# Optimization experiments

Hardware: AMD Instinct MI355X
Metric: run time of the kernel (lower is better)

Reference implementation:

```python
import jax, jax.numpy as jnp
import numpy as np

WS = 7            # window size
HEADS = 4
DIM = 128         # hidden_dim
HEAD_DIM = 128    # wrapper passes head_dim=hidden_dim (faithful to source)
INNER = HEADS * HEAD_DIM   # 512
MLP = 4 * DIM
PATCH = 4
DISP = WS // 2
NEG = -1e9


def _ln(x, g, b, eps=1e-5):
    m = jnp.mean(x, -1, keepdims=True)
    v = jnp.mean((x - m) ** 2, -1, keepdims=True)
    return (x - m) * jax.lax.rsqrt(v + eps) * g + b


_coords = np.stack(np.meshgrid(np.arange(WS), np.arange(WS), indexing='ij'), -1).reshape(-1, 2)
REL_IDX = jnp.asarray(_coords[None] - _coords[:, None] + WS - 1)  # (ws^2, ws^2, 2)


def _build_masks():
    n = WS * WS
    ul = np.zeros((n, n), np.float32)
    ul[-DISP * WS:, : -DISP * WS] = NEG
    ul[: -DISP * WS, -DISP * WS:] = NEG
    lr = np.zeros((WS, WS, WS, WS), np.float32)
    lr[:, -DISP:, :, : -DISP] = NEG
    lr[:, : -DISP, :, -DISP:] = NEG
    return jnp.asarray(ul), jnp.asarray(lr.reshape(n, n))

UL_MASK, LR_MASK = _build_masks()


def _win_attn(x, w_qkv, pos, w_o, b_o, shifted):
    b, H, W, _ = x.shape
    if shifted:
        x = jnp.roll(x, (-DISP, -DISP), axis=(1, 2))
    nh, nw = H // WS, W // WS
    qkv = x @ w_qkv  # (b, H, W, 3*INNER)

    def to_win(t):  # -> (b, heads, n_windows, ws*ws, head_dim)
        t = t.reshape(b, nh, WS, nw, WS, HEADS, HEAD_DIM)
        return t.transpose(0, 5, 1, 3, 2, 4, 6).reshape(b, HEADS, nh * nw, WS * WS, HEAD_DIM)

    q, k, v = map(to_win, jnp.split(qkv, 3, axis=-1))
    dots = jnp.einsum('bhwid,bhwjd->bhwij', q, k) * (HEAD_DIM ** -0.5)
    dots = dots + pos[REL_IDX[..., 0], REL_IDX[..., 1]]  # shared across heads (berniwal)
    if shifted:
        dots = dots.at[:, :, -nw:].add(UL_MASK)
        dots = dots.at[:, :, nw - 1::nw].add(LR_MASK)
    attn = jax.nn.softmax(dots, axis=-1)
    out = jnp.einsum('bhwij,bhwjd->bhwid', attn, v)
    out = out.reshape(b, HEADS, nh, nw, WS, WS, HEAD_DIM).transpose(0, 2, 4, 3, 5, 1, 6)
    out = out.reshape(b, H, W, INNER) @ w_o + b_o
    if shifted:
        out = jnp.roll(out, (DISP, DISP), axis=(1, 2))
    return out


def _block(x, ga1, be1, w_qkv, pos, w_o, b_o, ga2, be2, w1, b1, w2, b2, shifted):
    x = x + _win_attn(_ln(x, ga1, be1), w_qkv, pos, w_o, b_o, shifted)
    h = jax.nn.gelu(_ln(x, ga2, be2) @ w1 + b1, approximate=False) @ w2 + b2
    return x + h


def _patch_embed(x, w, b):  # Unfold(patch) + Linear, channel-major feature order
    B, C, H, W = x.shape
    nh, nw = H // PATCH, W // PATCH
    x = x.reshape(B, C, nh, PATCH, nw, PATCH).transpose(0, 2, 4, 1, 3, 5)
    return x.reshape(B, nh, nw, C * PATCH * PATCH) @ w + b


def setup_inputs() -> dict:
    key = jax.random.key(0)
    ks = iter(jax.random.split(key, 48))

    def nrm(shape, s=0.02):
        return jax.random.normal(next(ks), shape, dtype=jnp.float32) * s

    inp = {'x': jax.random.normal(next(ks), (32, 3, 224, 224), dtype=jnp.float32)}
    inp['w_pe'] = nrm((3 * PATCH * PATCH, DIM))
    inp['b_pe'] = jnp.zeros((DIM,), jnp.float32)
    for s in ('a', 'b'):
        inp['ga1_' + s] = jnp.ones((DIM,), jnp.float32)
        inp['be1_' + s] = jnp.zeros((DIM,), jnp.float32)
        inp['w_qkv_' + s] = nrm((DIM, 3 * INNER))
        inp['pos_' + s] = nrm((2 * WS - 1, 2 * WS - 1), 1.0)
        inp['w_o_' + s] = nrm((INNER, DIM))
        inp['b_o_' + s] = jnp.zeros((DIM,), jnp.float32)
        inp['ga2_' + s] = jnp.ones((DIM,), jnp.float32)
        inp['be2_' + s] = jnp.zeros((DIM,), jnp.float32)
        inp['w_m1_' + s] = nrm((DIM, MLP))
        inp['b_m1_' + s] = jnp.zeros((MLP,), jnp.float32)
        inp['w_m2_' + s] = nrm((MLP, DIM))
        inp['b_m2_' + s] = jnp.zeros((DIM,), jnp.float32)
    return inp


def reference(x, w_pe, b_pe,
              ga1_a, be1_a, w_qkv_a, pos_a, w_o_a, b_o_a, ga2_a, be2_a, w_m1_a, b_m1_a, w_m2_a, b_m2_a,
              ga1_b, be1_b, w_qkv_b, pos_b, w_o_b, b_o_b, ga2_b, be2_b, w_m1_b, b_m1_b, w_m2_b, b_m2_b):
    h = _patch_embed(x, w_pe, b_pe)  # (B, 56, 56, DIM)
    h = _block(h, ga1_a, be1_a, w_qkv_a, pos_a, w_o_a, b_o_a, ga2_a, be2_a, w_m1_a, b_m1_a, w_m2_a, b_m2_a, False)
    h = _block(h, ga1_b, be1_b, w_qkv_b, pos_b, w_o_b, b_o_b, ga2_b, be2_b, w_m1_b, b_m1_b, w_m2_b, b_m2_b, True)
    return h
```

## Files before the change

kernel.cpp:

```cpp
#include <hip/hip_runtime.h>

typedef __attribute__((ext_vector_type(8))) short bf16x8;
typedef __attribute__((ext_vector_type(4))) short bf16x4;
typedef __attribute__((ext_vector_type(4))) float f32x4;
typedef __attribute__((ext_vector_type(2))) unsigned u32x2;

#define MFMA16(a, b, c) __builtin_amdgcn_mfma_f32_16x16x32_bf16(a, b, c, 0, 0, 0)

static __device__ __forceinline__ short f2bf(float f) {
    union { float f; unsigned u; } x; x.f = f;
    unsigned r = x.u + 0x7FFFu + ((x.u >> 16) & 1u);
    return (short)(r >> 16);
}

static __device__ __forceinline__ unsigned cvtpk(float lo, float hi) {
    unsigned r;
    asm("v_cvt_pk_bf16_f32 %0, %1, %2" : "=v"(r) : "v"(lo), "v"(hi));
    return r;
}

static __device__ __forceinline__ void gload16(const void* g, void* l) {
    __builtin_amdgcn_global_load_lds((const __attribute__((address_space(1))) void*)g,
                                     (__attribute__((address_space(3))) void*)l, 16, 0, 0);
}

__global__ void wconv_kernel(const float* __restrict__ i_qkv, const float* __restrict__ i_o,
                             const float* __restrict__ i_m1, const float* __restrict__ i_m2,
                             short* __restrict__ wqkv, short* __restrict__ wo,
                             short* __restrict__ wm1, short* __restrict__ wm2) {
    int idx = blockIdx.x * 256 + threadIdx.x;
    if (idx < 196608) {
        int k = idx & 127, n = idx >> 7;
        wqkv[idx] = f2bf(i_qkv[k * 1536 + n]);
    } else if (idx < 262144) {
        int l = idx - 196608; int k = l & 511, n = l >> 9;
        wo[l] = f2bf(i_o[k * 128 + n]);
    } else if (idx < 327680) {
        int l = idx - 262144; int k = l & 127, n = l >> 7;
        wm1[l] = f2bf(i_m1[k * 512 + n]);
    } else {
        int l = idx - 327680; int k = l & 511, n = l >> 9;
        wm2[l] = f2bf(i_m2[k * 128 + n]);
    }
}

__global__ void tabgen_kernel(const float* __restrict__ pos_a, const float* __restrict__ pos_b,
                              float* __restrict__ tab) {
    int v = blockIdx.x;
    const float* pos = (v == 0) ? pos_a : pos_b;
    for (int e = threadIdx.x; e < 4096; e += 256) {
        int row = e >> 6, key = e & 63;
        float val;
        if (key >= 49) val = -1e9f;
        else if (row >= 49) val = 0.f;
        else {
            int qi = row / 7, qj = row - qi * 7, ki = key / 7, kj = key - ki * 7;
            val = pos[(ki - qi + 6) * 13 + (kj - qj + 6)];
            if (v >= 1) {
                bool wh7 = (v - 1) & 2, ww7 = (v - 1) & 1;
                if (wh7 && ((qi >= 4) != (ki >= 4))) val += -1e9f;
                if (ww7 && ((qj >= 4) != (kj >= 4))) val += -1e9f;
            }
        }
        tab[v * 4096 + e] = val;
    }
}

__global__ __launch_bounds__(256) void patchln_kernel(const float* __restrict__ x,
                                                      const float* __restrict__ w,
                                                      const float* __restrict__ bias,
                                                      const float* __restrict__ g,
                                                      const float* __restrict__ bta,
                                                      float* __restrict__ out,
                                                      short* __restrict__ xn) {
    __shared__ float s_in[2][48];
    __shared__ float red[2][2][2];
    const int tid = threadIdx.x;
    const int half = tid >> 7, c = tid & 127;
    const int winh = (tid >> 6) & 1, lane = tid & 63;
    const int t = blockIdx.x * 2 + half;
    const int b = t / 3136, rem = t - b * 3136;
    const int hp = rem / 56, wp = rem - hp * 56;
    if (c < 48) {
        int cin = c >> 4, py = (c >> 2) & 3, px = c & 3;
        s_in[half][c] = x[((size_t)(b * 3 + cin) * 224 + hp * 4 + py) * 224 + wp * 4 + px];
    }
    __syncthreads();
    float acc = bias[c];
#pragma unroll
    for (int k = 0; k < 48; ++k) acc += s_in[half][k] * w[k * 128 + c];
    out[(size_t)t * 128 + c] = acc;
    float s1 = acc, s2 = acc * acc;
#pragma unroll
    for (int o = 32; o > 0; o >>= 1) { s1 += __shfl_xor(s1, o); s2 += __shfl_xor(s2, o); }
    if (lane == 0) { red[half][winh][0] = s1; red[half][winh][1] = s2; }
    __syncthreads();
    s1 = red[half][0][0] + red[half][1][0];
    s2 = red[half][0][1] + red[half][1][1];
    float mean = s1 * (1.f / 128.f);
    float var = s2 * (1.f / 128.f) - mean * mean;
    float rstd = rsqrtf(var + 1e-5f);
    xn[(size_t)t * 128 + c] = f2bf((acc - mean) * rstd * g[c] + bta[c]);
}

template <int SHIFTED>
__global__ __launch_bounds__(256, 3) void attn_kernel(const short* __restrict__ xn,
                                                      const short* __restrict__ wqkvT,
                                                      const float* __restrict__ tab,
                                                      const short* __restrict__ zpad,
                                                      short* __restrict__ aout) {
    __shared__ short smem[24576];
    short* s_x = smem;
    short* s_q = smem + 8192;
    short* s_k = smem + 16384;
    short* s_vT = smem + 8192;
    short* s_p = smem + 16384;

    const int tid = threadIdx.x;
    const int wid = tid >> 6, lane = tid & 63;
    const int l15 = lane & 15, l4 = lane >> 4, klo = l4 * 8;
    const int bid = blockIdx.x;
    const int win = bid & 63, head = (bid >> 6) & 3, b = bid >> 8;
    const int wh = win >> 3, ww = win & 7;

#pragma unroll
    for (int it = 0; it < 4; ++it) {
        int slot = it * 256 + tid;
        int row = slot >> 4, scol = slot & 15;
        int colb = (scol * 16) ^ ((row & 7) << 4);
        const char* g;
        if (row < 49) {
            int wi = (row * 37) >> 8, wj = row - wi * 7;
            int hh = wh * 7 + wi, wp = ww * 7 + wj;
            if (SHIFTED) { hh += 3; if (hh >= 56) hh -= 56; wp += 3; if (wp >= 56) wp -= 56; }
            int t = (b * 56 + hh) * 56 + wp;
            g = (const char*)(xn + (size_t)t * 128) + colb;
        } else {
            g = (const char*)zpad + colb;
        }
        gload16(g, (char*)smem + (it * 256 + wid * 64) * 16);
    }
    __syncthreads();

    const f32x4 zero4 = {0.f, 0.f, 0.f, 0.f};

    {
        const short* Wq = wqkvT + (size_t)(head * 128) * 128;
        const short* Wk = wqkvT + (size_t)(512 + head * 128) * 128;
        f32x4 aq[2][4], ak[2][4];
#pragma unroll
        for (int mw = 0; mw < 2; ++mw)
#pragma unroll
            for (int j = 0; j < 4; ++j) { aq[mw][j] = zero4; ak[mw][j] = zero4; }
#pragma unroll
        for (int k0 = 0; k0 < 4; ++k0) {
            bf16x8 bx[4], awq[2], awk[2];
#pragma unroll
            for (int j = 0; j < 4; ++j) {
                int row = j * 16 + l15;
                bx[j] = *(const bf16x8*)((const char*)s_x + row * 256 + ((k0 * 64 + l4 * 16) ^ ((row & 7) << 4)));
            }
#pragma unroll
            for (int mw = 0; mw < 2; ++mw) {
                awq[mw] = *(const bf16x8*)(Wq + (size_t)(wid * 32 + mw * 16 + l15) * 128 + k0 * 32 + klo);
                awk[mw] = *(const bf16x8*)(Wk + (size_t)(wid * 32 + mw * 16 + l15) * 128 + k0 * 32 + klo);
            }
            __builtin_amdgcn_s_setprio(1);
#pragma unroll
            for (int mw = 0; mw < 2; ++mw)
#pragma unroll
                for (int j = 0; j < 4; ++j) {
                    aq[mw][j] = MFMA16(awq[mw], bx[j], aq[mw][j]);
                    ak[mw][j] = MFMA16(awk[mw], bx[j], ak[mw][j]);
                }
            __builtin_amdgcn_s_setprio(0);
        }
#pragma unroll
        for (int mw = 0; mw < 2; ++mw)
#pragma unroll
            for (int j = 0; j < 4; ++j) {
                u32x2 pq = { cvtpk(aq[mw][j][0], aq[mw][j][1]), cvtpk(aq[mw][j][2], aq[mw][j][3]) };
                u32x2 pk = { cvtpk(ak[mw][j][0], ak[mw][j][1]), cvtpk(ak[mw][j][2], ak[mw][j][3]) };
                int row = j * 16 + l15;
                int colb = (wid * 64 + mw * 32 + l4 * 8) ^ ((row & 7) << 4);
                *(u32x2*)((char*)s_q + row * 256 + colb) = pq;
                *(u32x2*)((char*)s_k + row * 256 + colb) = pk;
            }
    }
    __syncthreads();

    const int qrow = wid * 16 + l15;
    f32x4 dt[4];
#pragma unroll
    for (int m = 0; m < 4; ++m) dt[m] = zero4;
#pragma unroll
    for (int k0 = 0; k0 < 4; ++k0) {
        bf16x8 bq = *(const bf16x8*)((const char*)s_q + qrow * 256 + ((k0 * 64 + l4 * 16) ^ ((qrow & 7) << 4)));
        __builtin_amdgcn_s_setprio(1);
#pragma unroll
        for (int m = 0; m < 4; ++m) {
            int krow = m * 16 + l15;
            bf16x8 akf = *(const bf16x8*)((const char*)s_k + krow * 256 + ((k0 * 64 + l4 * 16) ^ ((krow & 7) << 4)));
            dt[m] = MFMA16(akf, bq, dt[m]);
        }
        __builtin_amdgcn_s_setprio(0);
    }
    __syncthreads();

    const int variant = SHIFTED ? (1 + ((wh == 7) ? 2 : 0) + ((ww == 7) ? 1 : 0)) : 0;
    const float* tv = tab + variant * 4096 + qrow * 64;
    const float SC = 0.08838834764831845f;
    float p[4][4];
    float mx = -3.0e38f;
#pragma unroll
    for (int m = 0; m < 4; ++m) {
        f32x4 tb = *(const f32x4*)(tv + m * 16 + l4 * 4);
#pragma unroll
        for (int r = 0; r < 4; ++r) {
            float d = dt[m][r] * SC + tb[r];
            p[m][r] = d;
            mx = fmaxf(mx, d);
        }
    }
    mx = fmaxf(mx, __shfl_xor(mx, 16));
    mx = fmaxf(mx, __shfl_xor(mx, 32));
    float sum = 0.f;
#pragma unroll
    for (int m = 0; m < 4; ++m)
#pragma unroll
        for (int r = 0; r < 4; ++r) { p[m][r] = __expf(p[m][r] - mx); sum += p[m][r]; }
    sum += __shfl_xor(sum, 16);
    sum += __shfl_xor(sum, 32);
    float inv = 1.f / sum;
#pragma unroll
    for (int m = 0; m < 4; ++m) {
        u32x2 pv = { cvtpk(p[m][0] * inv, p[m][1] * inv), cvtpk(p[m][2] * inv, p[m][3] * inv) };
        *(u32x2*)((char*)s_p + qrow * 128 + ((m * 32 + l4 * 8) ^ ((qrow & 7) << 4))) = pv;
    }

    {
        const short* Wv = wqkvT + (size_t)(1024 + head * 128) * 128;
        f32x4 acc[4][2];
#pragma unroll
        for (int m = 0; m < 4; ++m)
#pragma unroll
            for (int n = 0; n < 2; ++n) acc[m][n] = zero4;
#pragma unroll
        for (int k0 = 0; k0 < 4; ++k0) {
            bf16x8 ax[4], bw[2];
#pragma unroll
            for (int m = 0; m < 4; ++m) {
                int row = m * 16 + l15;
                ax[m] = *(const bf16x8*)((const char*)s_x + row * 256 + ((k0 * 64 + l4 * 16) ^ ((row & 7) << 4)));
            }
#pragma unroll
            for (int n = 0; n < 2; ++n)
                bw[n] = *(const bf16x8*)(Wv + (size_t)(wid * 32 + n * 16 + l15) * 128 + k0 * 32 + klo);
            __builtin_amdgcn_s_setprio(1);
#pragma unroll
            for (int m = 0; m < 4; ++m)
#pragma unroll
                for (int n = 0; n < 2; ++n) acc[m][n] = MFMA16(ax[m], bw[n], acc[m][n]);
            __builtin_amdgcn_s_setprio(0);
        }
#pragma unroll
        for (int m = 0; m < 4; ++m)
#pragma unroll
            for (int n = 0; n < 2; ++n) {
                u32x2 pv = { cvtpk(acc[m][n][0], acc[m][n][1]), cvtpk(acc[m][n][2], acc[m][n][3]) };
                int hd = wid * 32 + n * 16 + l15;
                *(u32x2*)((char*)s_vT + hd * 128 + ((m * 32 + l4 * 8) ^ ((hd & 7) << 4))) = pv;
            }
    }
    __syncthreads();

    f32x4 o[4][2];
#pragma unroll
    for (int m = 0; m < 4; ++m)
#pragma unroll
        for (int n = 0; n < 2; ++n) o[m][n] = zero4;
#pragma unroll
    for (int k0 = 0; k0 < 2; ++k0) {
        bf16x8 ap[4], bv[2];
#pragma unroll
        for (int m = 0; m < 4; ++m) {
            int row = m * 16 + l15;
            ap[m] = *(const bf16x8*)((const char*)s_p + row * 128 + ((k0 * 64 + l4 * 16) ^ ((row & 7) << 4)));
        }
#pragma unroll
        for (int n = 0; n < 2; ++n) {
            int hd = wid * 32 + n * 16 + l15;
            bv[n] = *(const bf16x8*)((const char*)s_vT + hd * 128 + ((k0 * 64 + l4 * 16) ^ ((hd & 7) << 4)));
        }
        __builtin_amdgcn_s_setprio(1);
#pragma unroll
        for (int m = 0; m < 4; ++m)
#pragma unroll
            for (int n = 0; n < 2; ++n) o[m][n] = MFMA16(ap[m], bv[n], o[m][n]);
        __builtin_amdgcn_s_setprio(0);
    }
#pragma unroll
    for (int m = 0; m < 4; ++m) {
#pragma unroll
        for (int r = 0; r < 4; ++r) {
            int rl = m * 16 + l4 * 4 + r;
            if (rl < 49) {
                int wi = (rl * 37) >> 8, wj = rl - wi * 7;
                int hh = wh * 7 + wi, wp = ww * 7 + wj;
                if (SHIFTED) { hh += 3; if (hh >= 56) hh -= 56; wp += 3; if (wp >= 56) wp -= 56; }
                size_t t = (size_t)(b * 56 + hh) * 56 + wp;
                aout[t * 512 + head * 128 + wid * 32 + l15] = f2bf(o[m][0][r]);
                aout[t * 512 + head * 128 + wid * 32 + 16 + l15] = f2bf(o[m][1][r]);
            }
        }
    }
}

template <int K, int MODE>
__global__ __launch_bounds__(256, 2) void gemm4_kernel(const short* __restrict__ A,
                                                       const short* __restrict__ BT,
                                                       const float* __restrict__ bias,
                                                       const float* __restrict__ resid,
                                                       const float* __restrict__ g,
                                                       const float* __restrict__ bta,
                                                       float* __restrict__ outf,
                                                       short* __restrict__ outb,
                                                       int Ntot) {
    __shared__ char smem[65536];
    float* red = (float*)smem;

    const int tid = threadIdx.x, wid = tid >> 6, lane = tid & 63;
    const int wr = wid >> 1, wc = wid & 1;
    const int l15 = lane & 15, l4 = lane >> 4;
    const int m0 = blockIdx.x * 128;
    const int nb0 = blockIdx.y * 128;

    auto stage = [&](int kc, int bi) {
#pragma unroll
        for (int it = 0; it < 4; ++it) {
            int slot = it * 256 + tid;
            int row = slot >> 3, scol = slot & 7;
            int colb = (scol * 16) ^ ((row & 7) << 4);
            gload16((const char*)(A + (size_t)(m0 + row) * K + kc * 64) + colb,
                    (char*)smem + bi * 32768 + (it * 256 + wid * 64) * 16);
        }
#pragma unroll
        for (int it = 0; it < 4; ++it) {
            int slot = it * 256 + tid;
            int row = slot >> 3, scol = slot & 7;
            int colb = (scol * 16) ^ ((row & 7) << 4);
            gload16((const char*)(BT + (size_t)(nb0 + row) * K + kc * 64) + colb,
                    (char*)smem + bi * 32768 + 16384 + (it * 256 + wid * 64) * 16);
        }
    };

    const f32x4 zero4 = {0.f, 0.f, 0.f, 0.f};
    f32x4 acc[4][4];
#pragma unroll
    for (int nf = 0; nf < 4; ++nf)
#pragma unroll
        for (int tm = 0; tm < 4; ++tm) acc[nf][tm] = zero4;

    stage(0, 0);
    __syncthreads();
    const int KC = K / 64;
#pragma unroll
    for (int kc = 0; kc < KC; ++kc) {
        if (kc + 1 < KC) stage(kc + 1, (kc + 1) & 1);
        const char* bufA = (const char*)smem + (kc & 1) * 32768;
        const char* bufB = bufA + 16384;
#pragma unroll
        for (int ks = 0; ks < 2; ++ks) {
            bf16x8 a[4], bfr[4];
#pragma unroll
            for (int tm = 0; tm < 4; ++tm) {
                int row = wr * 64 + tm * 16 + l15;
                a[tm] = *(const bf16x8*)(bufA + row * 128 + ((ks * 64 + l4 * 16) ^ ((row & 7) << 4)));
            }
#pragma unroll
            for (int nf = 0; nf < 4; ++nf) {
                int row = wc * 64 + nf * 16 + l15;
                bfr[nf] = *(const bf16x8*)(bufB + row * 128 + ((ks * 64 + l4 * 16) ^ ((row & 7) << 4)));
            }
            __builtin_amdgcn_s_setprio(1);
#pragma unroll
            for (int nf = 0; nf < 4; ++nf)
#pragma unroll
                for (int tm = 0; tm < 4; ++tm) acc[nf][tm] = MFMA16(bfr[nf], a[tm], acc[nf][tm]);
            __builtin_amdgcn_s_setprio(0);
        }
        __syncthreads();
    }

    f32x4 bv4[4];
#pragma unroll
    for (int nf = 0; nf < 4; ++nf)
        bv4[nf] = *(const f32x4*)(bias + nb0 + wc * 64 + nf * 16 + l4 * 4);

    if (MODE == 0) {
#pragma unroll
        for (int tm = 0; tm < 4; ++tm) {
            int row = m0 + wr * 64 + tm * 16 + l15;
#pragma unroll
            for (int nf = 0; nf < 4; ++nf) {
                float v[4];
#pragma unroll
                for (int r = 0; r < 4; ++r) {
                    float t = acc[nf][tm][r] + bv4[nf][r];
                    v[r] = 0.5f * t * (1.f + erff(t * 0.70710678118f));
                }
                u32x2 pv = { cvtpk(v[0], v[1]), cvtpk(v[2], v[3]) };
                *(u32x2*)(outb + (size_t)row * Ntot + nb0 + wc * 64 + nf * 16 + l4 * 4) = pv;
            }
        }
        return;
    }

    float s1[4], s2[4];
#pragma unroll
    for (int tm = 0; tm < 4; ++tm) {
        int row = m0 + wr * 64 + tm * 16 + l15;
        float a1 = 0.f, a2 = 0.f;
#pragma unroll
        for (int nf = 0; nf < 4; ++nf) {
            f32x4 rs = *(const f32x4*)(resid + (size_t)row * 128 + wc * 64 + nf * 16 + l4 * 4);
#pragma unroll
            for (int r = 0; r < 4; ++r) {
                float v = acc[nf][tm][r] + bv4[nf][r] + rs[r];
                acc[nf][tm][r] = v;
                a1 += v; a2 += v * v;
            }
        }
        s1[tm] = a1; s2[tm] = a2;
    }

    if (MODE == 1) {
#pragma unroll
        for (int tm = 0; tm < 4; ++tm) {
            s1[tm] += __shfl_xor(s1[tm], 16); s1[tm] += __shfl_xor(s1[tm], 32);
            s2[tm] += __shfl_xor(s2[tm], 16); s2[tm] += __shfl_xor(s2[tm], 32);
        }
        if (l4 == 0) {
#pragma unroll
            for (int tm = 0; tm < 4; ++tm) {
                int lrow = wr * 64 + tm * 16 + l15;
                red[lrow * 4 + wc * 2] = s1[tm];
                red[lrow * 4 + wc * 2 + 1] = s2[tm];
            }
        }
        __syncthreads();
    }

#pragma unroll
    for (int tm = 0; tm < 4; ++tm) {
        int lrow = wr * 64 + tm * 16 + l15;
        int row = m0 + lrow;
        float mean = 0.f, rstd = 0.f;
        if (MODE == 1) {
            f32x4 rd = *(const f32x4*)(red + lrow * 4);
            float t1 = rd[0] + rd[2], t2 = rd[1] + rd[3];
            mean = t1 * (1.f / 128.f);
            float var = t2 * (1.f / 128.f) - mean * mean;
            rstd = rsqrtf(var + 1e-5f);
        }
#pragma unroll
        for (int nf = 0; nf < 4; ++nf) {
            int col0 = wc * 64 + nf * 16 + l4 * 4;
            *(f32x4*)(outf + (size_t)row * 128 + col0) = acc[nf][tm];
            if (MODE == 1) {
                f32x4 gg = *(const f32x4*)(g + col0);
                f32x4 bb = *(const f32x4*)(bta + col0);
                float w0 = (acc[nf][tm][0] - mean) * rstd * gg[0] + bb[0];
                float w1 = (acc[nf][tm][1] - mean) * rstd * gg[1] + bb[1];
                float w2 = (acc[nf][tm][2] - mean) * rstd * gg[2] + bb[2];
                float w3 = (acc[nf][tm][3] - mean) * rstd * gg[3] + bb[3];
                u32x2 pb = { cvtpk(w0, w1), cvtpk(w2, w3) };
                *(u32x2*)(outb + (size_t)row * 128 + col0) = pb;
            }
        }
    }
}

extern "C" void kernel_launch(void* const* d_in, const int* in_sizes, int n_in,
                              void* d_out, int out_size, void* d_ws, size_t ws_size,
                              hipStream_t stream) {
    const float* x = (const float*)d_in[0];
    const float* w_pe = (const float*)d_in[1];
    const float* b_pe = (const float*)d_in[2];
    const float* P[24];
    for (int i = 0; i < 24; ++i) P[i] = (const float*)d_in[3 + i];

    float* out = (float*)d_out;
    const size_t TOK = 100352;

    short* xn = (short*)d_ws;
    short* abuf = xn + TOK * 128;
    short* wqkv = abuf + TOK * 512;
    short* wo = wqkv + 196608;
    short* wm1 = wo + 65536;
    short* wm2 = wm1 + 65536;
    float* tab = (float*)(wm2 + 65536);
    short* zpad = (short*)(tab + 5 * 4096);

    hipMemsetAsync(zpad, 0, 256, stream);
    tabgen_kernel<<<5, 256, 0, stream>>>(P[3], P[15], tab);

    patchln_kernel<<<50176, 256, 0, stream>>>(x, w_pe, b_pe, P[0], P[1], out, xn);

    for (int s = 0; s < 2; ++s) {
        wconv_kernel<<<1536, 256, 0, stream>>>(P[s * 12 + 2], P[s * 12 + 4], P[s * 12 + 8], P[s * 12 + 10],
                                               wqkv, wo, wm1, wm2);

        if (s == 0)
            attn_kernel<0><<<8192, 256, 0, stream>>>(xn, wqkv, tab, zpad, abuf);
        else
            attn_kernel<1><<<8192, 256, 0, stream>>>(xn, wqkv, tab, zpad, abuf);

        gemm4_kernel<512, 1><<<dim3(784, 1), 256, 0, stream>>>(
            abuf, wo, P[s * 12 + 5], out, P[s * 12 + 6], P[s * 12 + 7], out, xn, 128);

        gemm4_kernel<128, 0><<<dim3(784, 4), 256, 0, stream>>>(
            xn, wm1, P[s * 12 + 9], nullptr, nullptr, nullptr, nullptr, abuf, 512);

        if (s == 0)
            gemm4_kernel<512, 1><<<dim3(784, 1), 256, 0, stream>>>(
                abuf, wm2, P[11], out, P[12], P[13], out, xn, 128);
        else
            gemm4_kernel<512, 2><<<dim3(784, 1), 256, 0, stream>>>(
                abuf, wm2, P[23], out, nullptr, nullptr, out, nullptr, 128);
    }
}
```

Before: 621.8 us.

## Fuse output projection, LayerNorm and MLP first layer into one kernel

Merges the attention output projection (with residual and LN2) and the MLP up-projection with GELU into a single kernel. The normalized tile stays in shared memory as bf16 and feeds the hidden GEMM directly, so the xn round trip through global memory and one launch go away. The kernel writes hidden activations back into abuf, the same buffer it reads attention output from. That is safe only because each block reads just its own rows, and all of them are consumed before the writes start. The trade-offs are a per-block sequential loop over four hidden chunks with unpipelined weight loads, and lower parallelism than the 784x4 grid used before.

```diff
diff --git a/kernel.cpp b/kernel.cpp
--- a/kernel.cpp
+++ b/kernel.cpp
@@ -22,6 +22,10 @@
 static __device__ __forceinline__ void gload16(const void* g, void* l) {
     __builtin_amdgcn_global_load_lds((const __attribute__((address_space(1))) void*)g,
                                      (__attribute__((address_space(3))) void*)l, 16, 0, 0);
+}
+
+static __device__ __forceinline__ float gelu(float t) {
+    return 0.5f * t * (1.f + erff(t * 0.70710678118f));
 }
 
 __global__ void wconv_kernel(const float* __restrict__ i_qkv, const float* __restrict__ i_o,
@@ -316,24 +320,22 @@
     }
 }
 
-template <int K, int MODE>
-__global__ __launch_bounds__(256, 2) void gemm4_kernel(const short* __restrict__ A,
-                                                       const short* __restrict__ BT,
-                                                       const float* __restrict__ bias,
-                                                       const float* __restrict__ resid,
-                                                       const float* __restrict__ g,
-                                                       const float* __restrict__ bta,
-                                                       float* __restrict__ outf,
-                                                       short* __restrict__ outb,
-                                                       int Ntot) {
+__global__ __launch_bounds__(256, 2) void projmlp_kernel(const short* __restrict__ A,
+                                                         const short* __restrict__ woT,
+                                                         const short* __restrict__ wm1T,
+                                                         const float* __restrict__ b_o,
+                                                         const float* __restrict__ ga2,
+                                                         const float* __restrict__ be2,
+                                                         const float* __restrict__ b1,
+                                                         float* __restrict__ outf,
+                                                         short* __restrict__ hid) {
     __shared__ char smem[65536];
-    float* red = (float*)smem;
+    float* red = (float*)(smem + 32768);
 
     const int tid = threadIdx.x, wid = tid >> 6, lane = tid & 63;
     const int wr = wid >> 1, wc = wid & 1;
     const int l15 = lane & 15, l4 = lane >> 4;
     const int m0 = blockIdx.x * 128;
-    const int nb0 = blockIdx.y * 128;
 
     auto stage = [&](int kc, int bi) {
 #pragma unroll
@@ -341,7 +343,7 @@
             int slot = it * 256 + tid;
             int row = slot >> 3, scol = slot & 7;
             int colb = (scol * 16) ^ ((row & 7) << 4);
-            gload16((const char*)(A + (size_t)(m0 + row) * K + kc * 64) + colb,
+            gload16((const char*)(A + (size_t)(m0 + row) * 512 + kc * 64) + colb,
                     (char*)smem + bi * 32768 + (it * 256 + wid * 64) * 16);
         }
 #pragma unroll
@@ -349,7 +351,7 @@
             int slot = it * 256 + tid;
             int row = slot >> 3, scol = slot & 7;
             int colb = (scol * 16) ^ ((row & 7) << 4);
-            gload16((const char*)(BT + (size_t)(nb0 + row) * K + kc * 64) + colb,
+            gload16((const char*)(woT + (size_t)row * 512 + kc * 64) + colb,
                     (char*)smem + bi * 32768 + 16384 + (it * 256 + wid * 64) * 16);
         }
     };
@@ -363,10 +365,9 @@
 
     stage(0, 0);
     __syncthreads();
-    const int KC = K / 64;
-#pragma unroll
-    for (int kc = 0; kc < KC; ++kc) {
-        if (kc + 1 < KC) stage(kc + 1, (kc + 1) & 1);
+#pragma unroll
+    for (int kc = 0; kc < 8; ++kc) {
+        if (kc + 1 < 8) stage(kc + 1, (kc + 1) & 1);
         const char* bufA = (const char*)smem + (kc & 1) * 32768;
         const char* bufB = bufA + 16384;
 #pragma unroll
@@ -395,26 +396,7 @@
     f32x4 bv4[4];
 #pragma unroll
     for (int nf = 0; nf < 4; ++nf)
-        bv4[nf] = *(const f32x4*)(bias + nb0 + wc * 64 + nf * 16 + l4 * 4);
-
-    if (MODE == 0) {
-#pragma unroll
-        for (int tm = 0; tm < 4; ++tm) {
-            int row = m0 + wr * 64 + tm * 16 + l15;
-#pragma unroll
-            for (int nf = 0; nf < 4; ++nf) {
-                float v[4];
-#pragma unroll
-                for (int r = 0; r < 4; ++r) {
-                    float t = acc[nf][tm][r] + bv4[nf][r];
-                    v[r] = 0.5f * t * (1.f + erff(t * 0.70710678118f));
-                }
-                u32x2 pv = { cvtpk(v[0], v[1]), cvtpk(v[2], v[3]) };
-                *(u32x2*)(outb + (size_t)row * Ntot + nb0 + wc * 64 + nf * 16 + l4 * 4) = pv;
-            }
-        }
-        return;
-    }
+        bv4[nf] = *(const f32x4*)(b_o + wc * 64 + nf * 16 + l4 * 4);
 
     float s1[4], s2[4];
 #pragma unroll
@@ -423,7 +405,205 @@
         float a1 = 0.f, a2 = 0.f;
 #pragma unroll
         for (int nf = 0; nf < 4; ++nf) {
-            f32x4 rs = *(const f32x4*)(resid + (size_t)row * 128 + wc * 64 + nf * 16 + l4 * 4);
+            f32x4 rs = *(const f32x4*)(outf + (size_t)row * 128 + wc * 64 + nf * 16 + l4 * 4);
+#pragma unroll
+            for (int r = 0; r < 4; ++r) {
+                float v = acc[nf][tm][r] + bv4[nf][r] + rs[r];
+                acc[nf][tm][r] = v;
+                a1 += v; a2 += v * v;
+            }
+        }
+        s1[tm] = a1; s2[tm] = a2;
+    }
+#pragma unroll
+    for (int tm = 0; tm < 4; ++tm) {
+        s1[tm] += __shfl_xor(s1[tm], 16); s1[tm] += __shfl_xor(s1[tm], 32);
+        s2[tm] += __shfl_xor(s2[tm], 16); s2[tm] += __shfl_xor(s2[tm], 32);
+    }
+    if (l4 == 0) {
+#pragma unroll
+        for (int tm = 0; tm < 4; ++tm) {
+            int lrow = wr * 64 + tm * 16 + l15;
+            red[lrow * 4 + wc * 2] = s1[tm];
+            red[lrow * 4 + wc * 2 + 1] = s2[tm];
+        }
+    }
+    __syncthreads();
+
+    float mean[4], rstd[4];
+#pragma unroll
+    for (int tm = 0; tm < 4; ++tm) {
+        int lrow = wr * 64 + tm * 16 + l15;
+        f32x4 rd = *(const f32x4*)(red + lrow * 4);
+        float t1 = rd[0] + rd[2], t2 = rd[1] + rd[3];
+        mean[tm] = t1 * (1.f / 128.f);
+        float var = t2 * (1.f / 128.f) - mean[tm] * mean[tm];
+        rstd[tm] = rsqrtf(var + 1e-5f);
+    }
+    __syncthreads();
+
+#pragma unroll
+    for (int tm = 0; tm < 4; ++tm) {
+        int lrow = wr * 64 + tm * 16 + l15;
+        int row = m0 + lrow;
+#pragma unroll
+        for (int nf = 0; nf < 4; ++nf) {
+            int col0 = wc * 64 + nf * 16 + l4 * 4;
+            *(f32x4*)(outf + (size_t)row * 128 + col0) = acc[nf][tm];
+            f32x4 gg = *(const f32x4*)(ga2 + col0);
+            f32x4 bb = *(const f32x4*)(be2 + col0);
+            float w0 = (acc[nf][tm][0] - mean[tm]) * rstd[tm] * gg[0] + bb[0];
+            float w1 = (acc[nf][tm][1] - mean[tm]) * rstd[tm] * gg[1] + bb[1];
+            float w2 = (acc[nf][tm][2] - mean[tm]) * rstd[tm] * gg[2] + bb[2];
+            float w3 = (acc[nf][tm][3] - mean[tm]) * rstd[tm] * gg[3] + bb[3];
+            u32x2 pb = { cvtpk(w0, w1), cvtpk(w2, w3) };
+            *(u32x2*)((char*)smem + lrow * 256 + ((col0 * 2) ^ ((lrow & 7) << 4))) = pb;
+        }
+    }
+    __syncthreads();
+
+    for (int hc = 0; hc < 4; ++hc) {
+#pragma unroll
+        for (int it = 0; it < 8; ++it) {
+            int slot = it * 256 + tid;
+            int row = slot >> 4, scol = slot & 15;
+            int colb = (scol * 16) ^ ((row & 7) << 4);
+            gload16((const char*)(wm1T + (size_t)(hc * 128 + row) * 128) + colb,
+                    (char*)smem + 32768 + (it * 256 + wid * 64) * 16);
+        }
+        __syncthreads();
+
+#pragma unroll
+        for (int nf = 0; nf < 4; ++nf)
+#pragma unroll
+            for (int tm = 0; tm < 4; ++tm) acc[nf][tm] = zero4;
+#pragma unroll
+        for (int ks = 0; ks < 4; ++ks) {
+            bf16x8 a[4], bfr[4];
+#pragma unroll
+            for (int tm = 0; tm < 4; ++tm) {
+                int row = wr * 64 + tm * 16 + l15;
+                a[tm] = *(const bf16x8*)((const char*)smem + row * 256 + ((ks * 64 + l4 * 16) ^ ((row & 7) << 4)));
+            }
+#pragma unroll
+            for (int nf = 0; nf < 4; ++nf) {
+                int hrow = wc * 64 + nf * 16 + l15;
+                bfr[nf] = *(const bf16x8*)((const char*)smem + 32768 + hrow * 256 + ((ks * 64 + l4 * 16) ^ ((hrow & 7) << 4)));
+            }
+            __builtin_amdgcn_s_setprio(1);
+#pragma unroll
+            for (int nf = 0; nf < 4; ++nf)
+#pragma unroll
+                for (int tm = 0; tm < 4; ++tm) acc[nf][tm] = MFMA16(bfr[nf], a[tm], acc[nf][tm]);
+            __builtin_amdgcn_s_setprio(0);
+        }
+
+        f32x4 b14[4];
+#pragma unroll
+        for (int nf = 0; nf < 4; ++nf)
+            b14[nf] = *(const f32x4*)(b1 + hc * 128 + wc * 64 + nf * 16 + l4 * 4);
+#pragma unroll
+        for (int tm = 0; tm < 4; ++tm) {
+            int row = m0 + wr * 64 + tm * 16 + l15;
+#pragma unroll
+            for (int nf = 0; nf < 4; ++nf) {
+                float v0 = gelu(acc[nf][tm][0] + b14[nf][0]);
+                float v1 = gelu(acc[nf][tm][1] + b14[nf][1]);
+                float v2 = gelu(acc[nf][tm][2] + b14[nf][2]);
+                float v3 = gelu(acc[nf][tm][3] + b14[nf][3]);
+                u32x2 pv = { cvtpk(v0, v1), cvtpk(v2, v3) };
+                *(u32x2*)(hid + (size_t)row * 512 + hc * 128 + wc * 64 + nf * 16 + l4 * 4) = pv;
+            }
+        }
+        __syncthreads();
+    }
+}
+
+template <int MODE>
+__global__ __launch_bounds__(256, 2) void gemm4_kernel(const short* __restrict__ A,
+                                                       const short* __restrict__ BT,
+                                                       const float* __restrict__ bias,
+                                                       const float* __restrict__ g,
+                                                       const float* __restrict__ bta,
+                                                       float* __restrict__ outf,
+                                                       short* __restrict__ outb) {
+    __shared__ char smem[65536];
+    float* red = (float*)smem;
+
+    const int tid = threadIdx.x, wid = tid >> 6, lane = tid & 63;
+    const int wr = wid >> 1, wc = wid & 1;
+    const int l15 = lane & 15, l4 = lane >> 4;
+    const int m0 = blockIdx.x * 128;
+
+    auto stage = [&](int kc, int bi) {
+#pragma unroll
+        for (int it = 0; it < 4; ++it) {
+            int slot = it * 256 + tid;
+            int row = slot >> 3, scol = slot & 7;
+            int colb = (scol * 16) ^ ((row & 7) << 4);
+            gload16((const char*)(A + (size_t)(m0 + row) * 512 + kc * 64) + colb,
+                    (char*)smem + bi * 32768 + (it * 256 + wid * 64) * 16);
+        }
+#pragma unroll
+        for (int it = 0; it < 4; ++it) {
+            int slot = it * 256 + tid;
+            int row = slot >> 3, scol = slot & 7;
+            int colb = (scol * 16) ^ ((row & 7) << 4);
+            gload16((const char*)(BT + (size_t)row * 512 + kc * 64) + colb,
+                    (char*)smem + bi * 32768 + 16384 + (it * 256 + wid * 64) * 16);
+        }
+    };
+
+    const f32x4 zero4 = {0.f, 0.f, 0.f, 0.f};
+    f32x4 acc[4][4];
+#pragma unroll
+    for (int nf = 0; nf < 4; ++nf)
+#pragma unroll
+        for (int tm = 0; tm < 4; ++tm) acc[nf][tm] = zero4;
+
+    stage(0, 0);
+    __syncthreads();
+#pragma unroll
+    for (int kc = 0; kc < 8; ++kc) {
+        if (kc + 1 < 8) stage(kc + 1, (kc + 1) & 1);
+        const char* bufA = (const char*)smem + (kc & 1) * 32768;
+        const char* bufB = bufA + 16384;
+#pragma unroll
+        for (int ks = 0; ks < 2; ++ks) {
+            bf16x8 a[4], bfr[4];
+#pragma unroll
+            for (int tm = 0; tm < 4; ++tm) {
+                int row = wr * 64 + tm * 16 + l15;
+                a[tm] = *(const bf16x8*)(bufA + row * 128 + ((ks * 64 + l4 * 16) ^ ((row & 7) << 4)));
+            }
+#pragma unroll
+            for (int nf = 0; nf < 4; ++nf) {
+                int row = wc * 64 + nf * 16 + l15;
+                bfr[nf] = *(const bf16x8*)(bufB + row * 128 + ((ks * 64 + l4 * 16) ^ ((row & 7) << 4)));
+            }
+            __builtin_amdgcn_s_setprio(1);
+#pragma unroll
+            for (int nf = 0; nf < 4; ++nf)
+#pragma unroll
+                for (int tm = 0; tm < 4; ++tm) acc[nf][tm] = MFMA16(bfr[nf], a[tm], acc[nf][tm]);
+            __builtin_amdgcn_s_setprio(0);
+        }
+        __syncthreads();
+    }
+
+    f32x4 bv4[4];
+#pragma unroll
+    for (int nf = 0; nf < 4; ++nf)
+        bv4[nf] = *(const f32x4*)(bias + wc * 64 + nf * 16 + l4 * 4);
+
+    float s1[4], s2[4];
+#pragma unroll
+    for (int tm = 0; tm < 4; ++tm) {
+        int row = m0 + wr * 64 + tm * 16 + l15;
+        float a1 = 0.f, a2 = 0.f;
+#pragma unroll
+        for (int nf = 0; nf < 4; ++nf) {
+            f32x4 rs = *(const f32x4*)(outf + (size_t)row * 128 + wc * 64 + nf * 16 + l4 * 4);
 #pragma unroll
             for (int r = 0; r < 4; ++r) {
                 float v = acc[nf][tm][r] + bv4[nf][r] + rs[r];
@@ -516,17 +696,14 @@
         else
             attn_kernel<1><<<8192, 256, 0, stream>>>(xn, wqkv, tab, zpad, abuf);
 
-        gemm4_kernel<512, 1><<<dim3(784, 1), 256, 0, stream>>>(
-            abuf, wo, P[s * 12 + 5], out, P[s * 12 + 6], P[s * 12 + 7], out, xn, 128);
-
-        gemm4_kernel<128, 0><<<dim3(784, 4), 256, 0, stream>>>(
-            xn, wm1, P[s * 12 + 9], nullptr, nullptr, nullptr, nullptr, abuf, 512);
+        projmlp_kernel<<<784, 256, 0, stream>>>(
+            abuf, wo, wm1, P[s * 12 + 5], P[s * 12 + 6], P[s * 12 + 7], P[s * 12 + 9], out, abuf);
 
         if (s == 0)
-            gemm4_kernel<512, 1><<<dim3(784, 1), 256, 0, stream>>>(
-                abuf, wm2, P[11], out, P[12], P[13], out, xn, 128);
+            gemm4_kernel<1><<<784, 256, 0, stream>>>(
+                abuf, wm2, P[11], P[12], P[13], out, xn);
         else
-            gemm4_kernel<512, 2><<<dim3(784, 1), 256, 0, stream>>>(
-                abuf, wm2, P[23], out, nullptr, nullptr, out, nullptr, 128);
-    }
-}
+            gemm4_kernel<2><<<784, 256, 0, stream>>>(
+                abuf, wm2, P[23], nullptr, nullptr, out, nullptr);
+    }
+}
```

Result: faster. 594.3 us (-4.4%).
